# Optimization experiments

Measured on AMD Instinct MI355X. Metric: run time of the kernel, lower is better.

Reference implementation:

```python
import jax, jax.numpy as jnp
import numpy as np

N = 100000
E = 1600000
D_IN = 64
D_HID = 64


def gcn_layer(x, W, b, src, dst, n):
    # PyG GCNConv: h = D^{-1/2} (A + I) D^{-1/2} (x W) + b
    h = x @ W                                   # [N, d_out]
    deg = jnp.zeros((n,), x.dtype).at[dst].add(1.0) + 1.0  # in-degree + self loop
    dinv = jax.lax.rsqrt(deg)                   # deg >= 1 so safe
    norm = dinv[src] * dinv[dst]                # [E]
    msg = h[src] * norm[:, None]                # gather + scale, [E, d_out]
    out = jax.ops.segment_sum(msg, dst, num_segments=n)  # scatter-add
    out = out + h * (dinv * dinv)[:, None]      # self-loop term
    return out + b


def setup_inputs() -> dict:
    key = jax.random.key(0)
    ks = jax.random.split(key, 8)
    x = jax.random.normal(ks[0], (N, D_IN), dtype=jnp.float32)
    edge_index = jax.random.randint(ks[1], (2, E), 0, N, dtype=jnp.int64)
    s = 1.0 / np.sqrt(D_IN)
    W1 = jax.random.uniform(ks[2], (D_IN, D_HID), jnp.float32, -s, s)
    b1 = jnp.zeros((D_HID,), jnp.float32)
    s2 = 1.0 / np.sqrt(D_HID)
    W2 = jax.random.uniform(ks[3], (D_HID, D_HID), jnp.float32, -s2, s2)
    b2 = jnp.zeros((D_HID,), jnp.float32)
    W3 = jax.random.uniform(ks[4], (D_HID, 1), jnp.float32, -s2, s2)
    b3 = jnp.zeros((1,), jnp.float32)
    return {"x": x, "edge_index": edge_index, "W1": W1, "b1": b1,
            "W2": W2, "b2": b2, "W3": W3, "b3": b3}


def reference(x, edge_index, W1, b1, W2, b2, W3, b3):
    src, dst = edge_index[0], edge_index[1]
    n = x.shape[0]
    # dropout(p=0.1) is identity in eval mode
    h = jax.nn.relu(gcn_layer(x, W1, b1, src, dst, n))
    h = jax.nn.relu(gcn_layer(h, W2, b2, src, dst, n))
    out = gcn_layer(h, W3, b3, src, dst, n)     # [N, 1]
    return out
```

## Files before the change

kernel.cpp:

```cpp
#include <hip/hip_runtime.h>


#define THREADS 256
#define NPB_SHIFT 9
#define NPB 512
#define BCAP 9216
#define STAGE_CAP 9216

__global__ __launch_bounds__(THREADS) void k_bscat2(
    const int* __restrict__ src, const int* __restrict__ dst,
    int* __restrict__ bucketCur, int* __restrict__ eb, int E) {
  __shared__ int hist[4][256];
  __shared__ int hcur[256];
  int t = threadIdx.x;
  for (int j = t; j < 1024; j += THREADS) ((int*)hist)[j] = 0;
  __syncthreads();
  int blockStart = blockIdx.x * 4096;
  int sub = t & 3;
#pragma unroll
  for (int c = 0; c < 4; c++) {
    int e0 = blockStart + c * 1024 + t * 4;
    if (e0 + 3 < E) {
      int4 d = *(const int4*)(dst + e0);
      atomicAdd(&hist[sub][d.x >> NPB_SHIFT], 1);
      atomicAdd(&hist[sub][d.y >> NPB_SHIFT], 1);
      atomicAdd(&hist[sub][d.z >> NPB_SHIFT], 1);
      atomicAdd(&hist[sub][d.w >> NPB_SHIFT], 1);
    } else {
      int lim = min(e0 + 4, E);
      for (int e = e0; e < lim; e++) atomicAdd(&hist[sub][dst[e] >> NPB_SHIFT], 1);
    }
  }
  __syncthreads();
  int cnt = hist[0][t] + hist[1][t] + hist[2][t] + hist[3][t];
  int rb = 0;
  if (cnt) rb = atomicAdd(&bucketCur[t], cnt);
  __syncthreads();
  hcur[t] = rb;
  __syncthreads();
#pragma unroll
  for (int c = 0; c < 4; c++) {
    int e0 = blockStart + c * 1024 + t * 4;
    if (e0 + 3 < E) {
      int4 s = *(const int4*)(src + e0);
      int4 d = *(const int4*)(dst + e0);
      int b, q;
      b = d.x >> NPB_SHIFT; q = atomicAdd(&hcur[b], 1);
      eb[b * BCAP + q] = ((d.x & (NPB - 1)) << 17) | s.x;
      b = d.y >> NPB_SHIFT; q = atomicAdd(&hcur[b], 1);
      eb[b * BCAP + q] = ((d.y & (NPB - 1)) << 17) | s.y;
      b = d.z >> NPB_SHIFT; q = atomicAdd(&hcur[b], 1);
      eb[b * BCAP + q] = ((d.z & (NPB - 1)) << 17) | s.z;
      b = d.w >> NPB_SHIFT; q = atomicAdd(&hcur[b], 1);
      eb[b * BCAP + q] = ((d.w & (NPB - 1)) << 17) | s.w;
    } else {
      int lim = min(e0 + 4, E);
      for (int e = e0; e < lim; e++) {
        int dd = dst[e];
        int b = dd >> NPB_SHIFT;
        int q = atomicAdd(&hcur[b], 1);
        eb[b * BCAP + q] = ((dd & (NPB - 1)) << 17) | src[e];
      }
    }
  }
}

__global__ __launch_bounds__(THREADS) void k_bscan2(
    const int* __restrict__ bucketCur, int* __restrict__ bucketOff,
    int* __restrict__ rowptr, int n, int E, int nbuck) {
  __shared__ int sh[THREADS];
  int t = threadIdx.x;
  int v = (t < nbuck) ? bucketCur[t] : 0;
  sh[t] = v;
  __syncthreads();
  for (int off = 1; off < THREADS; off <<= 1) {
    int u = (t >= off) ? sh[t - off] : 0;
    __syncthreads();
    sh[t] += u;
    __syncthreads();
  }
  bucketOff[t] = sh[t] - v;
  if (t == 0) {
    bucketOff[nbuck] = E;
    rowptr[n] = E;
  }
}

__global__ __launch_bounds__(THREADS) void k_bcsr3(
    const int* __restrict__ eb, const int* __restrict__ bucketCur,
    const int* __restrict__ bucketOff, int* __restrict__ rowptr,
    float* __restrict__ dinv, int* __restrict__ es, int n) {
  __shared__ int lcnt4[4][NPB];
  __shared__ int lcnt[NPB];
  __shared__ int sA[NPB];
  __shared__ int sB[NPB];
  __shared__ int lcur[NPB];
  __shared__ int stage[STAGE_CAP];
  int b = blockIdx.x;
  int t = threadIdx.x;
  int cntB = bucketCur[b];
  int baseIn = b * BCAP;
  int baseOut = bucketOff[b];
  int node0 = b << NPB_SHIFT;
  int nn = min(NPB, n - node0);
  int sub = t & 3;

  for (int j = t; j < 4 * NPB; j += THREADS) ((int*)lcnt4)[j] = 0;
  __syncthreads();
  for (int p = t; p < cntB; p += THREADS) {
    int v = eb[baseIn + p];
    atomicAdd(&lcnt4[sub][v >> 17], 1);
  }
  __syncthreads();
#pragma unroll
  for (int k = 0; k < 2; k++) {
    int j = t + k * 256;
    lcnt[j] = lcnt4[0][j] + lcnt4[1][j] + lcnt4[2][j] + lcnt4[3][j];
  }
  __syncthreads();
  sA[t] = lcnt[t]; sA[t + 256] = lcnt[t + 256];
  __syncthreads();
  int* bin = sA; int* bout = sB;
  for (int off = 1; off < NPB; off <<= 1) {
    int j0 = t, j1 = t + 256;
    int a0 = bin[j0] + ((j0 >= off) ? bin[j0 - off] : 0);
    int a1 = bin[j1] + ((j1 >= off) ? bin[j1 - off] : 0);
    bout[j0] = a0; bout[j1] = a1;
    __syncthreads();
    int* tmp = bin; bin = bout; bout = tmp;
  }
#pragma unroll
  for (int k = 0; k < 2; k++) {
    int j = t + k * 256;
    if (j < nn) {
      int c = lcnt[j];
      int ex = bin[j] - c;
      rowptr[node0 + j] = baseOut + ex;
      dinv[node0 + j] = rsqrtf((float)c + 1.f);
      lcur[j] = ex;
    }
  }
  __syncthreads();
  for (int p = t; p < cntB; p += THREADS) {
    int v = eb[baseIn + p];
    int q = atomicAdd(&lcur[v >> 17], 1);
    if (q < STAGE_CAP) stage[q] = v & 0x1FFFF;
  }
  __syncthreads();
  int lim = min(cntB, STAGE_CAP);
  for (int q = t; q < lim; q += THREADS) es[baseOut + q] = stage[q];
}

__global__ __launch_bounds__(THREADS) void k_gemmT(
    const float* __restrict__ A, const float* __restrict__ W,
    const float* __restrict__ dinv, float* __restrict__ C, int n) {
  __shared__ float At[16 * 64];
  int t = threadIdx.x;
  int lane = t & 63;
  int wid = t >> 6;

  float w[64];
#pragma unroll
  for (int k = 0; k < 64; k++) w[k] = W[k * 64 + lane];

  int ntiles = (n + 15) >> 4;
  for (int tile = blockIdx.x; tile < ntiles; tile += gridDim.x) {
    int row0 = tile << 4;
    {
      int r = row0 + (t >> 4);
      float4 v = make_float4(0.f, 0.f, 0.f, 0.f);
      if (r < n) v = ((const float4*)(A + (size_t)row0 * 64))[t];
      ((float4*)At)[t] = v;
    }
    __syncthreads();

#pragma unroll
    for (int j = 0; j < 4; j++) {
      int lr = wid * 4 + j;
      int r = row0 + lr;
      float acc0 = 0.f, acc1 = 0.f, acc2 = 0.f, acc3 = 0.f;
#pragma unroll
      for (int q = 0; q < 4; q++) {
        float4 a0 = *(const float4*)&At[lr * 64 + q * 16 + 0];
        float4 a1 = *(const float4*)&At[lr * 64 + q * 16 + 4];
        float4 a2 = *(const float4*)&At[lr * 64 + q * 16 + 8];
        float4 a3 = *(const float4*)&At[lr * 64 + q * 16 + 12];
        int k0 = q * 16;
        acc0 = fmaf(a0.x, w[k0 + 0],  acc0);
        acc1 = fmaf(a0.y, w[k0 + 1],  acc1);
        acc2 = fmaf(a0.z, w[k0 + 2],  acc2);
        acc3 = fmaf(a0.w, w[k0 + 3],  acc3);
        acc0 = fmaf(a1.x, w[k0 + 4],  acc0);
        acc1 = fmaf(a1.y, w[k0 + 5],  acc1);
        acc2 = fmaf(a1.z, w[k0 + 6],  acc2);
        acc3 = fmaf(a1.w, w[k0 + 7],  acc3);
        acc0 = fmaf(a2.x, w[k0 + 8],  acc0);
        acc1 = fmaf(a2.y, w[k0 + 9],  acc1);
        acc2 = fmaf(a2.z, w[k0 + 10], acc2);
        acc3 = fmaf(a2.w, w[k0 + 11], acc3);
        acc0 = fmaf(a3.x, w[k0 + 12], acc0);
        acc1 = fmaf(a3.y, w[k0 + 13], acc1);
        acc2 = fmaf(a3.z, w[k0 + 14], acc2);
        acc3 = fmaf(a3.w, w[k0 + 15], acc3);
      }
      if (r < n)
        C[(size_t)r * 64 + lane] = ((acc0 + acc1) + (acc2 + acc3)) * dinv[r];
    }
    __syncthreads();
  }
}

template <int MODE>
__global__ __launch_bounds__(THREADS) void k_agg64f(
    const float* __restrict__ hs, const float* __restrict__ dinv,
    const int* __restrict__ rowptr, const int* __restrict__ es,
    const float* __restrict__ b, const float* __restrict__ Wn,
    float* __restrict__ out, int n) {
  __shared__ float rowbuf[4][64];
  int t = threadIdx.x;
  int lane = t & 63;
  int g = lane >> 4;
  int c = lane & 15;
  int wid = t >> 6;
  int gw = (int)((blockIdx.x * THREADS + t) >> 6);
  int nw = (gridDim.x * THREADS) >> 6;
  const float4* h4 = (const float4*)hs;
  float4 bb = ((const float4*)b)[c];

  float w[MODE == 1 ? 64 : 1];
  if (MODE == 1) {
#pragma unroll
    for (int k = 0; k < 64; k++) w[k] = Wn[k * 64 + lane];
  } else {
    w[0] = Wn[lane];
  }

  for (int i = gw; i < n; i += nw) {
    int p1 = rowptr[i + 1];
    int p = rowptr[i] + g;
    float4 acc  = make_float4(0.f, 0.f, 0.f, 0.f);
    float4 acc1 = make_float4(0.f, 0.f, 0.f, 0.f);
    float4 acc2 = make_float4(0.f, 0.f, 0.f, 0.f);
    float4 acc3 = make_float4(0.f, 0.f, 0.f, 0.f);
    for (; p + 12 < p1; p += 16) {
      int s0 = es[p];
      int s1 = es[p + 4];
      int s2 = es[p + 8];
      int s3 = es[p + 12];
      float4 v0 = h4[(size_t)s0 * 16 + c];
      float4 v1 = h4[(size_t)s1 * 16 + c];
      float4 v2 = h4[(size_t)s2 * 16 + c];
      float4 v3 = h4[(size_t)s3 * 16 + c];
      acc.x  += v0.x; acc.y  += v0.y; acc.z  += v0.z; acc.w  += v0.w;
      acc1.x += v1.x; acc1.y += v1.y; acc1.z += v1.z; acc1.w += v1.w;
      acc2.x += v2.x; acc2.y += v2.y; acc2.z += v2.z; acc2.w += v2.w;
      acc3.x += v3.x; acc3.y += v3.y; acc3.z += v3.z; acc3.w += v3.w;
    }
    for (; p + 4 < p1; p += 8) {
      int s0 = es[p];
      int s1 = es[p + 4];
      float4 v0 = h4[(size_t)s0 * 16 + c];
      float4 v1 = h4[(size_t)s1 * 16 + c];
      acc.x  += v0.x; acc.y  += v0.y; acc.z  += v0.z; acc.w  += v0.w;
      acc1.x += v1.x; acc1.y += v1.y; acc1.z += v1.z; acc1.w += v1.w;
    }
    if (p < p1) {
      int s0 = es[p];
      float4 v0 = h4[(size_t)s0 * 16 + c];
      acc.x += v0.x; acc.y += v0.y; acc.z += v0.z; acc.w += v0.w;
    }
    acc.x += acc1.x + acc2.x + acc3.x;
    acc.y += acc1.y + acc2.y + acc3.y;
    acc.z += acc1.z + acc2.z + acc3.z;
    acc.w += acc1.w + acc2.w + acc3.w;
#pragma unroll
    for (int m = 16; m <= 32; m <<= 1) {
      acc.x += __shfl_xor(acc.x, m, 64);
      acc.y += __shfl_xor(acc.y, m, 64);
      acc.z += __shfl_xor(acc.z, m, 64);
      acc.w += __shfl_xor(acc.w, m, 64);
    }
    float di = dinv[i];
    if (g == 0) {
      float4 self = h4[(size_t)i * 16 + c];
      float4 a;
      a.x = fmaxf(di * (acc.x + self.x) + bb.x, 0.f);
      a.y = fmaxf(di * (acc.y + self.y) + bb.y, 0.f);
      a.z = fmaxf(di * (acc.z + self.z) + bb.z, 0.f);
      a.w = fmaxf(di * (acc.w + self.w) + bb.w, 0.f);
      *(float4*)&rowbuf[wid][c * 4] = a;
    }
    if (MODE == 1) {
      const float* rb = rowbuf[wid];
      float o0 = 0.f, o1 = 0.f, o2 = 0.f, o3 = 0.f;
#pragma unroll
      for (int q = 0; q < 4; q++) {
        float4 a0 = *(const float4*)&rb[q * 16 + 0];
        float4 a1 = *(const float4*)&rb[q * 16 + 4];
        float4 a2 = *(const float4*)&rb[q * 16 + 8];
        float4 a3 = *(const float4*)&rb[q * 16 + 12];
        int k0 = q * 16;
        o0 = fmaf(a0.x, w[k0 + 0],  o0);
        o1 = fmaf(a0.y, w[k0 + 1],  o1);
        o2 = fmaf(a0.z, w[k0 + 2],  o2);
        o3 = fmaf(a0.w, w[k0 + 3],  o3);
        o0 = fmaf(a1.x, w[k0 + 4],  o0);
        o1 = fmaf(a1.y, w[k0 + 5],  o1);
        o2 = fmaf(a1.z, w[k0 + 6],  o2);
        o3 = fmaf(a1.w, w[k0 + 7],  o3);
        o0 = fmaf(a2.x, w[k0 + 8],  o0);
        o1 = fmaf(a2.y, w[k0 + 9],  o1);
        o2 = fmaf(a2.z, w[k0 + 10], o2);
        o3 = fmaf(a2.w, w[k0 + 11], o3);
        o0 = fmaf(a3.x, w[k0 + 12], o0);
        o1 = fmaf(a3.y, w[k0 + 13], o1);
        o2 = fmaf(a3.z, w[k0 + 14], o2);
        o3 = fmaf(a3.w, w[k0 + 15], o3);
      }
      out[(size_t)i * 64 + lane] = ((o0 + o1) + (o2 + o3)) * di;
    } else {
      float v = rowbuf[wid][lane] * w[0];
#pragma unroll
      for (int m = 1; m < 64; m <<= 1) v += __shfl_xor(v, m, 64);
      if (lane == 0) out[i] = v * di;
    }
  }
}

__global__ __launch_bounds__(THREADS) void k_agg1(
    const float* __restrict__ g3, const float* __restrict__ dinv,
    const int* __restrict__ rowptr, const int* __restrict__ es,
    const float* __restrict__ b3, float* __restrict__ out, int n) {
  int i = blockIdx.x * blockDim.x + threadIdx.x;
  if (i >= n) return;
  int p = rowptr[i], p1 = rowptr[i + 1];
  float acc = 0.f, accb = 0.f;
  for (; p + 1 < p1; p += 2) {
    acc  += g3[es[p]];
    accb += g3[es[p + 1]];
  }
  if (p < p1) acc += g3[es[p]];
  out[i] = dinv[i] * (acc + accb + g3[i]) + b3[0];
}

extern "C" void kernel_launch(void* const* d_in, const int* in_sizes, int n_in,
                              void* d_out, int out_size, void* d_ws, size_t ws_size,
                              hipStream_t stream) {
  const float* x  = (const float*)d_in[0];
  const int*   ei = (const int*)d_in[1];
  const float* W1 = (const float*)d_in[2];
  const float* b1 = (const float*)d_in[3];
  const float* W2 = (const float*)d_in[4];
  const float* b2 = (const float*)d_in[5];
  const float* W3 = (const float*)d_in[6];
  const float* b3 = (const float*)d_in[7];
  float* out = (float*)d_out;

  const int n = in_sizes[0] / 64;
  const int E = in_sizes[1] / 2;
  const int* src = ei;
  const int* dst = ei + E;
  const int nbuck = (n + NPB - 1) >> NPB_SHIFT;
  const int nA = (E + 4095) / 4096;

  char* w = (char*)d_ws;
  auto alloc = [&](size_t bytes) -> void* {
    void* p = (void*)w;
    w += (bytes + 255) & ~(size_t)255;
    return p;
  };
  int*   bucketCur = (int*)alloc(256 * 4);
  int*   bucketOff = (int*)alloc(257 * 4);
  int*   rowptr    = (int*)alloc(((size_t)n + 1) * 4);
  int*   eb        = (int*)alloc((size_t)256 * BCAP * 4);
  int*   es        = (int*)alloc((size_t)E * 4);
  float* dinv      = (float*)alloc((size_t)n * 4);
  float* g3        = (float*)alloc((size_t)n * 4);
  float* bufA      = (float*)alloc((size_t)n * 64 * 4);
  float* bufB      = (float*)alloc((size_t)n * 64 * 4);

  const int gN    = (n + THREADS - 1) / THREADS;
  const int gGemm = 1024;
  const int gAgg  = 2048;

  hipMemsetAsync(bucketCur, 0, 256 * 4, stream);
  k_bscat2<<<nA, THREADS, 0, stream>>>(src, dst, bucketCur, eb, E);
  k_bscan2<<<1, THREADS, 0, stream>>>(bucketCur, bucketOff, rowptr, n, E, nbuck);
  k_bcsr3<<<nbuck, THREADS, 0, stream>>>(eb, bucketCur, bucketOff, rowptr, dinv, es, n);

  k_gemmT<<<gGemm, THREADS, 0, stream>>>(x, W1, dinv, bufA, n);
  k_agg64f<1><<<gAgg, THREADS, 0, stream>>>(bufA, dinv, rowptr, es, b1, W2, bufB, n);
  k_agg64f<2><<<gAgg, THREADS, 0, stream>>>(bufB, dinv, rowptr, es, b2, W3, g3, n);
  k_agg1<<<gN, THREADS, 0, stream>>>(g3, dinv, rowptr, es, b3, out, n);
}
```

Before: 224.0 us.

## Keep W2 in shared memory and broadcast activations via shuffles in agg kernel

The fused aggregate+transform kernel used to hold a 64-entry per-lane register array of W and pass each activated row through a shared rowbuf. Now W2 is staged once per block in 16KB of shared memory, and each lane shuffles the activated row values to the others for the 64x64 matvec. The layer-3 dot product now runs on each lane's float4 with a 4-step shuffle reduction instead of a 6-step one. The aim is to cut VGPR pressure and raise occupancy for this gather-bound kernel, at the cost of more LDS reads and shuffles per row.

```diff
diff --git a/kernel.cpp b/kernel.cpp
--- a/kernel.cpp
+++ b/kernel.cpp
@@ -216,24 +216,25 @@
     const int* __restrict__ rowptr, const int* __restrict__ es,
     const float* __restrict__ b, const float* __restrict__ Wn,
     float* __restrict__ out, int n) {
-  __shared__ float rowbuf[4][64];
+  __shared__ float W2s[MODE == 1 ? 64 * 64 : 64];
   int t = threadIdx.x;
   int lane = t & 63;
   int g = lane >> 4;
   int c = lane & 15;
-  int wid = t >> 6;
   int gw = (int)((blockIdx.x * THREADS + t) >> 6);
   int nw = (gridDim.x * THREADS) >> 6;
   const float4* h4 = (const float4*)hs;
   float4 bb = ((const float4*)b)[c];
 
-  float w[MODE == 1 ? 64 : 1];
   if (MODE == 1) {
-#pragma unroll
-    for (int k = 0; k < 64; k++) w[k] = Wn[k * 64 + lane];
-  } else {
-    w[0] = Wn[lane];
-  }
+    const float4* Wn4 = (const float4*)Wn;
+    float4* W2s4 = (float4*)W2s;
+#pragma unroll
+    for (int j = 0; j < 4; j++) W2s4[t + j * 256] = Wn4[t + j * 256];
+    __syncthreads();
+  }
+  float4 w3 = make_float4(0.f, 0.f, 0.f, 0.f);
+  if (MODE == 2) w3 = ((const float4*)Wn)[c];
 
   for (int i = gw; i < n; i += nw) {
     int p1 = rowptr[i + 1];
@@ -281,47 +282,33 @@
       acc.w += __shfl_xor(acc.w, m, 64);
     }
     float di = dinv[i];
-    if (g == 0) {
-      float4 self = h4[(size_t)i * 16 + c];
-      float4 a;
-      a.x = fmaxf(di * (acc.x + self.x) + bb.x, 0.f);
-      a.y = fmaxf(di * (acc.y + self.y) + bb.y, 0.f);
-      a.z = fmaxf(di * (acc.z + self.z) + bb.z, 0.f);
-      a.w = fmaxf(di * (acc.w + self.w) + bb.w, 0.f);
-      *(float4*)&rowbuf[wid][c * 4] = a;
-    }
+    float4 self = h4[(size_t)i * 16 + c];
+    float4 a;
+    a.x = fmaxf(di * (acc.x + self.x) + bb.x, 0.f);
+    a.y = fmaxf(di * (acc.y + self.y) + bb.y, 0.f);
+    a.z = fmaxf(di * (acc.z + self.z) + bb.z, 0.f);
+    a.w = fmaxf(di * (acc.w + self.w) + bb.w, 0.f);
+
     if (MODE == 1) {
-      const float* rb = rowbuf[wid];
       float o0 = 0.f, o1 = 0.f, o2 = 0.f, o3 = 0.f;
 #pragma unroll
-      for (int q = 0; q < 4; q++) {
-        float4 a0 = *(const float4*)&rb[q * 16 + 0];
-        float4 a1 = *(const float4*)&rb[q * 16 + 4];
-        float4 a2 = *(const float4*)&rb[q * 16 + 8];
-        float4 a3 = *(const float4*)&rb[q * 16 + 12];
-        int k0 = q * 16;
-        o0 = fmaf(a0.x, w[k0 + 0],  o0);
-        o1 = fmaf(a0.y, w[k0 + 1],  o1);
-        o2 = fmaf(a0.z, w[k0 + 2],  o2);
-        o3 = fmaf(a0.w, w[k0 + 3],  o3);
-        o0 = fmaf(a1.x, w[k0 + 4],  o0);
-        o1 = fmaf(a1.y, w[k0 + 5],  o1);
-        o2 = fmaf(a1.z, w[k0 + 6],  o2);
-        o3 = fmaf(a1.w, w[k0 + 7],  o3);
-        o0 = fmaf(a2.x, w[k0 + 8],  o0);
-        o1 = fmaf(a2.y, w[k0 + 9],  o1);
-        o2 = fmaf(a2.z, w[k0 + 10], o2);
-        o3 = fmaf(a2.w, w[k0 + 11], o3);
-        o0 = fmaf(a3.x, w[k0 + 12], o0);
-        o1 = fmaf(a3.y, w[k0 + 13], o1);
-        o2 = fmaf(a3.z, w[k0 + 14], o2);
-        o3 = fmaf(a3.w, w[k0 + 15], o3);
+      for (int k4 = 0; k4 < 16; k4++) {
+        float a0 = __shfl(a.x, k4, 64);
+        float a1 = __shfl(a.y, k4, 64);
+        float a2 = __shfl(a.z, k4, 64);
+        float a3 = __shfl(a.w, k4, 64);
+        o0 = fmaf(a0, W2s[(4 * k4 + 0) * 64 + lane], o0);
+        o1 = fmaf(a1, W2s[(4 * k4 + 1) * 64 + lane], o1);
+        o2 = fmaf(a2, W2s[(4 * k4 + 2) * 64 + lane], o2);
+        o3 = fmaf(a3, W2s[(4 * k4 + 3) * 64 + lane], o3);
       }
       out[(size_t)i * 64 + lane] = ((o0 + o1) + (o2 + o3)) * di;
     } else {
-      float v = rowbuf[wid][lane] * w[0];
-#pragma unroll
-      for (int m = 1; m < 64; m <<= 1) v += __shfl_xor(v, m, 64);
+      float v = a.x * w3.x + a.y * w3.y + a.z * w3.z + a.w * w3.w;
+      v += __shfl_xor(v, 1, 64);
+      v += __shfl_xor(v, 2, 64);
+      v += __shfl_xor(v, 4, 64);
+      v += __shfl_xor(v, 8, 64);
       if (lane == 0) out[i] = v * di;
     }
   }
```

New measurement: 259.6 us. +15.9%, slower.
